# Kernel tuning notes

Measured on AMD Instinct MI355X. Metric: run time of the kernel, lower is better.

The kernel has to match this reference:

```python
import jax, jax.numpy as jnp
import numpy as np

N_NODES = 50000
N_EDGES = 800000
IN_CH = 128
CH = 128
OUT_CH = 128
N_TAPS = 3
N_LAYERS = 2


def setup_inputs() -> dict:
    key = jax.random.key(0)
    ks = jax.random.split(key, 8)
    s = 0.05
    x = jax.random.normal(ks[0], (N_NODES, IN_CH), dtype=jnp.float32)
    edge_index = jax.random.randint(ks[1], (2, N_EDGES), 0, N_NODES)
    # readin MLP: 1 layer, plain_last=False -> Linear + activation
    w_in = jax.random.normal(ks[2], (IN_CH, CH), dtype=jnp.float32) * s
    b_in = jnp.zeros((CH,), jnp.float32)
    # per-layer GraphFilter taps: (n_taps+1) Linears of [CH, CH]
    taps_w = jax.random.normal(ks[3], (N_LAYERS, N_TAPS + 1, CH, CH), dtype=jnp.float32) * s
    taps_b = jax.random.normal(ks[4], (N_LAYERS, N_TAPS + 1, CH), dtype=jnp.float32) * s
    # readout MLP: 1 layer, plain_last=True -> Linear only
    w_out = jax.random.normal(ks[5], (CH, OUT_CH), dtype=jnp.float32) * s
    b_out = jnp.zeros((OUT_CH,), jnp.float32)
    return {
        "x": x,
        "edge_index": edge_index,
        "w_in": w_in,
        "b_in": b_in,
        "taps_w": taps_w,
        "taps_b": taps_b,
        "w_out": w_out,
        "b_out": b_out,
    }


def reference(x, edge_index, w_in, b_in, taps_w, taps_b, w_out, b_out):
    act = jax.nn.leaky_relu  # torch LeakyReLU default negative_slope=0.01
    src, dst = edge_index[0], edge_index[1]
    n = x.shape[0]

    # readin: Linear + act (plain_last=False)
    h = act(x @ w_in + b_in)

    n_layers, n_taps_p1 = taps_w.shape[0], taps_w.shape[1]
    for l in range(n_layers):
        # ResidualBlock: y = act(h); y = GraphFilter(y); h = h + y
        y = act(h)
        out = y @ taps_w[l, 0] + taps_b[l, 0]
        for k in range(1, n_taps_p1):
            # SimpleConv(aggr='sum'): y_i = sum_{(s->i) in E} y_s
            y = jax.ops.segment_sum(y[src], dst, num_segments=n)
            out = out + y @ taps_w[l, k] + taps_b[l, k]
        h = h + out

    # readout: Linear only (plain_last=True)
    return h @ w_out + b_out
```

## Files before the change

### kernel.cpp

```cpp
#include <hip/hip_runtime.h>

typedef unsigned int uint;
typedef unsigned short ushort;

using bf16x8 = __attribute__((ext_vector_type(8))) short;
using f32x4  = __attribute__((ext_vector_type(4))) float;

__device__ __forceinline__ float lrelu(float v) { return v > 0.f ? v : 0.01f * v; }
__device__ __forceinline__ float b2f(ushort u) { return __uint_as_float((uint)u << 16); }
__device__ __forceinline__ ushort f2b(float f) {
  uint u = __float_as_uint(f);
  u += 0x7fffu + ((u >> 16) & 1u);
  return (ushort)(u >> 16);
}

#define CSR_B 256
#define BKT_SHIFT 10
#define MAX_NB 64

template <int MODE, int K>
__global__ __launch_bounds__(256) void gemm_mfma(
    const ushort* __restrict__ A0, const ushort* __restrict__ A1,
    const ushort* __restrict__ A2, const ushort* __restrict__ A3,
    const ushort* __restrict__ Wt, const float* __restrict__ bias,
    float* __restrict__ h, ushort* __restrict__ yout, int do_act, int N) {
  __shared__ ushort As[64][40];
  __shared__ ushort Bs[128][40];
  const int tid = threadIdx.x;
  const int lane = tid & 63;
  const int wave = tid >> 6;
  const int g = lane >> 4;
  const int mr = lane & 15;
  const int wr = wave >> 1;
  const int wc = wave & 1;
  const int row0 = blockIdx.x * 64;

  const ushort* Ap[4] = {A0, A1, A2, A3};

  f32x4 acc[2][4];
#pragma unroll
  for (int i = 0; i < 2; i++)
#pragma unroll
    for (int j = 0; j < 4; j++) acc[i][j] = (f32x4){0.f, 0.f, 0.f, 0.f};

#pragma unroll 4
  for (int kc = 0; kc < K; kc += 32) {
    {
      int m = tid >> 2, q = tid & 3;
      int r = row0 + m;
      if (r >= N) r = N - 1;
      int kg = kc + q * 8;
      const ushort* ap = Ap[kg >> 7] + (size_t)r * 128 + (kg & 127);
      *(uint4*)&As[m][q * 8] = *(const uint4*)ap;
    }
#pragma unroll
    for (int t = 0; t < 2; t++) {
      int slot = tid + t * 256;
      int n = slot >> 2, q = slot & 3;
      *(uint4*)&Bs[n][q * 8] = *(const uint4*)(Wt + (size_t)n * K + kc + q * 8);
    }
    __syncthreads();
    bf16x8 af[2], bf[4];
#pragma unroll
    for (int rt = 0; rt < 2; rt++) af[rt] = *(bf16x8*)&As[wr * 32 + rt * 16 + mr][g * 8];
#pragma unroll
    for (int ct = 0; ct < 4; ct++) bf[ct] = *(bf16x8*)&Bs[wc * 64 + ct * 16 + mr][g * 8];
#pragma unroll
    for (int rt = 0; rt < 2; rt++)
#pragma unroll
      for (int ct = 0; ct < 4; ct++)
        acc[rt][ct] = __builtin_amdgcn_mfma_f32_16x16x32_bf16(af[rt], bf[ct], acc[rt][ct], 0, 0, 0);
    __syncthreads();
  }

#pragma unroll
  for (int rt = 0; rt < 2; rt++) {
#pragma unroll
    for (int i = 0; i < 4; i++) {
      int R = row0 + wr * 32 + rt * 16 + g * 4 + i;
      if (R >= N) continue;
#pragma unroll
      for (int ct = 0; ct < 4; ct++) {
        int c = wc * 64 + ct * 16 + mr;
        float v = acc[rt][ct][i] + bias[c];
        size_t o = (size_t)R * 128 + c;
        if (MODE == 0) {
          float hv = lrelu(v);
          h[o] = hv;
          yout[o] = f2b(lrelu(hv));
        } else if (MODE == 1) {
          float hv = h[o] + v;
          h[o] = hv;
          if (yout) yout[o] = f2b(do_act ? lrelu(hv) : hv);
        } else {
          h[o] = v;
        }
      }
    }
  }
}

__global__ __launch_bounds__(256) void agg_bf16(const ushort* __restrict__ yin,
                                                ushort* __restrict__ yout,
                                                const int* __restrict__ rowp,
                                                const ushort* __restrict__ esrc, int N) {
  int t = threadIdx.x;
  int node = blockIdx.x * 16 + (t >> 4);
  if (node >= N) return;
  int lane = t & 15;
  int beg = rowp[node], end = rowp[node + 1];
  float s[8] = {0.f, 0.f, 0.f, 0.f, 0.f, 0.f, 0.f, 0.f};
  int j = beg;
  for (; j + 4 <= end; j += 4) {
    int s0 = esrc[j], s1 = esrc[j + 1], s2 = esrc[j + 2], s3 = esrc[j + 3];
    union { uint4 v; ushort u[8]; } w0, w1, w2, w3;
    w0.v = *(const uint4*)(yin + (size_t)s0 * 128 + lane * 8);
    w1.v = *(const uint4*)(yin + (size_t)s1 * 128 + lane * 8);
    w2.v = *(const uint4*)(yin + (size_t)s2 * 128 + lane * 8);
    w3.v = *(const uint4*)(yin + (size_t)s3 * 128 + lane * 8);
#pragma unroll
    for (int e = 0; e < 8; e++)
      s[e] += (b2f(w0.u[e]) + b2f(w1.u[e])) + (b2f(w2.u[e]) + b2f(w3.u[e]));
  }
  for (; j < end; j++) {
    int sn = esrc[j];
    union { uint4 v; ushort u[8]; } w;
    w.v = *(const uint4*)(yin + (size_t)sn * 128 + lane * 8);
#pragma unroll
    for (int e = 0; e < 8; e++) s[e] += b2f(w.u[e]);
  }
  union { uint4 v; ushort u[8]; } o;
#pragma unroll
  for (int e = 0; e < 8; e++) o.u[e] = f2b(s[e]);
  *(uint4*)(yout + (size_t)node * 128 + lane * 8) = o.v;
}

__global__ __launch_bounds__(256) void cast_f2b(const float* __restrict__ in,
                                                ushort* __restrict__ out, int n8) {
  int i = blockIdx.x * 256 + threadIdx.x;
  if (i >= n8) return;
  float4 a = ((const float4*)in)[i * 2];
  float4 b = ((const float4*)in)[i * 2 + 1];
  float v[8] = {a.x, a.y, a.z, a.w, b.x, b.y, b.z, b.w};
  union { uint4 q; ushort u[8]; } o;
#pragma unroll
  for (int e = 0; e < 8; e++) o.u[e] = f2b(v[e]);
  ((uint4*)out)[i] = o.q;
}

__global__ __launch_bounds__(256) void prep_k(const float* __restrict__ w_in,
                                              const float* __restrict__ w_out,
                                              const float* __restrict__ taps_w,
                                              const float* __restrict__ taps_b,
                                              ushort* __restrict__ Wt_in,
                                              ushort* __restrict__ Wt_out,
                                              ushort* __restrict__ Wt_l0,
                                              ushort* __restrict__ Wt_l1,
                                              float* __restrict__ bsum) {
  int gid = blockIdx.x * 256 + threadIdx.x;
  if (gid < 16384) {
    int n = gid >> 7, k = gid & 127;
    Wt_in[gid] = f2b(w_in[k * 128 + n]);
  } else if (gid < 32768) {
    int i = gid - 16384;
    int n = i >> 7, k = i & 127;
    Wt_out[i] = f2b(w_out[k * 128 + n]);
  } else if (gid < 98304) {
    int i = gid - 32768;
    int n = i >> 9, k = i & 511;
    Wt_l0[i] = f2b(taps_w[(size_t)k * 128 + n]);
  } else if (gid < 163840) {
    int i = gid - 98304;
    int n = i >> 9, k = i & 511;
    Wt_l1[i] = f2b(taps_w[(size_t)(512 + k) * 128 + n]);
  } else if (gid < 164096) {
    int i = gid - 163840;
    int l = i >> 7, n = i & 127;
    float s = 0.f;
    for (int k = 0; k < 4; k++) s += taps_b[l * 512 + k * 128 + n];
    bsum[i] = s;
  }
}

__global__ __launch_bounds__(256) void chist_k(const int* __restrict__ dst,
                                               int* __restrict__ H, int E, int NB) {
  __shared__ int hh[MAX_NB];
  if (threadIdx.x < NB) hh[threadIdx.x] = 0;
  __syncthreads();
  int chunk = (E + gridDim.x - 1) / gridDim.x;
  int beg = blockIdx.x * chunk, end = min(E, beg + chunk);
  for (int e = beg + threadIdx.x; e < end; e += 256)
    atomicAdd(&hh[dst[e] >> BKT_SHIFT], 1);
  __syncthreads();
  if (threadIdx.x < NB) H[threadIdx.x * gridDim.x + blockIdx.x] = hh[threadIdx.x];
}

__global__ __launch_bounds__(256) void cscan_k(int* __restrict__ H, int M) {
  __shared__ int sm[256];
  int per = (M + 255) / 256;
  int b0 = threadIdx.x * per;
  int hi = min(M, b0 + per);
  int sum = 0;
  for (int i = b0; i < hi; i++) sum += H[i];
  sm[threadIdx.x] = sum;
  __syncthreads();
  int x = sum;
  for (int off = 1; off < 256; off <<= 1) {
    int tt = (threadIdx.x >= off) ? sm[threadIdx.x - off] : 0;
    __syncthreads();
    x += tt;
    sm[threadIdx.x] = x;
    __syncthreads();
  }
  int run = x - sum;
  for (int i = b0; i < hi; i++) {
    int v = H[i];
    H[i] = run;
    run += v;
  }
}

__global__ __launch_bounds__(256) void cscatter_k(const int* __restrict__ src,
                                                  const int* __restrict__ dst,
                                                  const int* __restrict__ H,
                                                  uint* __restrict__ packed,
                                                  int E, int NB) {
  __shared__ int cur[MAX_NB];
  int chunk = (E + gridDim.x - 1) / gridDim.x;
  int beg = blockIdx.x * chunk, end = min(E, beg + chunk);
  if (threadIdx.x < NB) cur[threadIdx.x] = H[threadIdx.x * gridDim.x + blockIdx.x];
  __syncthreads();
  for (int e = beg + threadIdx.x; e < end; e += 256) {
    int d = dst[e];
    int pos = atomicAdd(&cur[d >> BKT_SHIFT], 1);
    packed[pos] = ((uint)d << 16) | (uint)src[e];
  }
}

__global__ __launch_bounds__(256) void fsort_k(const uint* __restrict__ packed,
                                               const int* __restrict__ H,
                                               ushort* __restrict__ esrc,
                                               int* __restrict__ rowp,
                                               int N, int E, int NB) {
  __shared__ int hist[1 << BKT_SHIFT];
  __shared__ int cur[1 << BKT_SHIFT];
  __shared__ int sm[256];
  const int bkt = blockIdx.x;
  const int base = bkt << BKT_SHIFT;
  const int nb_nodes = min(1 << BKT_SHIFT, N - base);
  const int start = H[bkt * CSR_B];
  const int end = (bkt == NB - 1) ? E : H[(bkt + 1) * CSR_B];

  for (int i = threadIdx.x; i < (1 << BKT_SHIFT); i += 256) hist[i] = 0;
  __syncthreads();
  for (int e = start + threadIdx.x; e < end; e += 256)
    atomicAdd(&hist[(packed[e] >> 16) - base], 1);
  __syncthreads();

  int t4 = threadIdx.x * 4;
  int l0 = hist[t4], l1 = hist[t4 + 1], l2 = hist[t4 + 2], l3 = hist[t4 + 3];
  int ssum = l0 + l1 + l2 + l3;
  sm[threadIdx.x] = ssum;
  __syncthreads();
  int x = ssum;
  for (int off = 1; off < 256; off <<= 1) {
    int tt = (threadIdx.x >= off) ? sm[threadIdx.x - off] : 0;
    __syncthreads();
    x += tt;
    sm[threadIdx.x] = x;
    __syncthreads();
  }
  int c0 = start + x - ssum;
  int c1 = c0 + l0, c2 = c1 + l1, c3 = c2 + l2;
  cur[t4] = c0; cur[t4 + 1] = c1; cur[t4 + 2] = c2; cur[t4 + 3] = c3;
  if (t4 + 0 < nb_nodes) rowp[base + t4 + 0] = c0;
  if (t4 + 1 < nb_nodes) rowp[base + t4 + 1] = c1;
  if (t4 + 2 < nb_nodes) rowp[base + t4 + 2] = c2;
  if (t4 + 3 < nb_nodes) rowp[base + t4 + 3] = c3;
  __syncthreads();

  for (int e = start + threadIdx.x; e < end; e += 256) {
    uint p = packed[e];
    int pos = atomicAdd(&cur[(p >> 16) - base], 1);
    esrc[pos] = (ushort)(p & 0xffffu);
  }
  if (bkt == 0 && threadIdx.x == 0) rowp[N] = E;
}

extern "C" void kernel_launch(void* const* d_in, const int* in_sizes, int n_in,
                              void* d_out, int out_size, void* d_ws, size_t ws_size,
                              hipStream_t stream) {
  const float* x      = (const float*)d_in[0];
  const int*   ei     = (const int*)d_in[1];
  const float* w_in   = (const float*)d_in[2];
  const float* b_in   = (const float*)d_in[3];
  const float* taps_w = (const float*)d_in[4];
  const float* taps_b = (const float*)d_in[5];
  const float* w_out  = (const float*)d_in[6];
  const float* b_out  = (const float*)d_in[7];

  const int N = in_sizes[0] / 128;
  const int E = in_sizes[1] / 2;
  const int* src = ei;
  const int* dst = ei + E;
  const int NB = (N + (1 << BKT_SHIFT) - 1) >> BKT_SHIFT;

  float* h = (float*)d_out;

  const size_t yelem = (size_t)N * 128;
  ushort* y0 = (ushort*)d_ws;
  ushort* y1 = y0 + yelem;
  ushort* y2 = y1 + yelem;
  ushort* y3 = y2 + yelem;
  ushort* Wt_in  = y3 + yelem;
  ushort* Wt_out = Wt_in + 128 * 128;
  ushort* Wt_l0  = Wt_out + 128 * 128;
  ushort* Wt_l1  = Wt_l0 + 128 * 512;
  float*  bsum   = (float*)(Wt_l1 + 128 * 512);
  int*    rowp   = (int*)(bsum + 256);
  int*    H      = rowp + (N + 1);
  uint*   packed = (uint*)(H + MAX_NB * CSR_B);
  ushort* esrc   = (ushort*)(packed + E);

  const int gemmB = (N + 63) / 64;
  const int aggB  = (N + 15) / 16;
  const int castB = (N * 16 + 255) / 256;

  chist_k<<<CSR_B, 256, 0, stream>>>(dst, H, E, NB);
  cscan_k<<<1, 256, 0, stream>>>(H, NB * CSR_B);
  cscatter_k<<<CSR_B, 256, 0, stream>>>(src, dst, H, packed, E, NB);
  fsort_k<<<NB, 256, 0, stream>>>(packed, H, esrc, rowp, N, E, NB);

  prep_k<<<641, 256, 0, stream>>>(w_in, w_out, taps_w, taps_b,
                                  Wt_in, Wt_out, Wt_l0, Wt_l1, bsum);
  cast_f2b<<<castB, 256, 0, stream>>>(x, y1, N * 16);

  gemm_mfma<0, 128><<<gemmB, 256, 0, stream>>>(y1, y1, y1, y1, Wt_in, b_in, h, y0, 0, N);

  for (int l = 0; l < 2; l++) {
    const ushort* Wt_l = (l == 0) ? Wt_l0 : Wt_l1;
    agg_bf16<<<aggB, 256, 0, stream>>>(y0, y1, rowp, esrc, N);
    agg_bf16<<<aggB, 256, 0, stream>>>(y1, y2, rowp, esrc, N);
    agg_bf16<<<aggB, 256, 0, stream>>>(y2, y3, rowp, esrc, N);
    gemm_mfma<1, 512><<<gemmB, 256, 0, stream>>>(y0, y1, y2, y3, Wt_l, bsum + l * 128,
                                                 h, y0, (l == 0) ? 1 : 0, N);
  }

  gemm_mfma<2, 128><<<gemmB, 256, 0, stream>>>(y0, y0, y0, y0, Wt_out, b_out,
                                               (float*)d_out, nullptr, 0, N);
}
```

Measured before the change: 410.0 us.

## Store bf16 node features in chunk-major 16-channel layout for cache-local gathers

Node feature buffers are reorganised from row-major [N][128] into eight chunk-major planes of [N][16], and the aggregation kernel assigns each block one channel chunk with 4 threads per node. The goal is to shrink the per-pass random-gather working set so it fits in on-chip caches. GEMM loads/stores and the input cast are adapted to the new layout. The trade-off is narrower 8-byte per-lane gathers and 32-byte row segments, which may waste cache-line bandwidth, and blocks of different chunks are interleaved rather than grouped.

```diff
diff --git a/kernel.cpp b/kernel.cpp
--- a/kernel.cpp
+++ b/kernel.cpp
@@ -17,6 +17,7 @@
 #define CSR_B 256
 #define BKT_SHIFT 10
 #define MAX_NB 64
+
 
 template <int MODE, int K>
 __global__ __launch_bounds__(256) void gemm_mfma(
@@ -50,7 +51,8 @@
       int r = row0 + m;
       if (r >= N) r = N - 1;
       int kg = kc + q * 8;
-      const ushort* ap = Ap[kg >> 7] + (size_t)r * 128 + (kg & 127);
+      const ushort* ap = Ap[kg >> 7] + ((size_t)((kg >> 4) & 7)) * N * 16 +
+                         (size_t)r * 16 + (kg & 15);
       *(uint4*)&As[m][q * 8] = *(const uint4*)ap;
     }
 #pragma unroll
@@ -84,14 +86,15 @@
         int c = wc * 64 + ct * 16 + mr;
         float v = acc[rt][ct][i] + bias[c];
         size_t o = (size_t)R * 128 + c;
+        size_t oy = (size_t)(wc * 4 + ct) * N * 16 + (size_t)R * 16 + mr;
         if (MODE == 0) {
           float hv = lrelu(v);
           h[o] = hv;
-          yout[o] = f2b(lrelu(hv));
+          yout[oy] = f2b(lrelu(hv));
         } else if (MODE == 1) {
           float hv = h[o] + v;
           h[o] = hv;
-          if (yout) yout[o] = f2b(do_act ? lrelu(hv) : hv);
+          if (yout) yout[oy] = f2b(do_act ? lrelu(hv) : hv);
         } else {
           h[o] = v;
         }
@@ -105,47 +108,51 @@
                                                 const int* __restrict__ rowp,
                                                 const ushort* __restrict__ esrc, int N) {
   int t = threadIdx.x;
-  int node = blockIdx.x * 16 + (t >> 4);
+  int chunk = blockIdx.x & 7;
+  int node = (blockIdx.x >> 3) * 64 + (t >> 2);
   if (node >= N) return;
-  int lane = t & 15;
+  int lane = t & 3;
+  const ushort* yb = yin + (size_t)chunk * N * 16 + lane * 4;
   int beg = rowp[node], end = rowp[node + 1];
-  float s[8] = {0.f, 0.f, 0.f, 0.f, 0.f, 0.f, 0.f, 0.f};
+  float s[4] = {0.f, 0.f, 0.f, 0.f};
   int j = beg;
   for (; j + 4 <= end; j += 4) {
     int s0 = esrc[j], s1 = esrc[j + 1], s2 = esrc[j + 2], s3 = esrc[j + 3];
-    union { uint4 v; ushort u[8]; } w0, w1, w2, w3;
-    w0.v = *(const uint4*)(yin + (size_t)s0 * 128 + lane * 8);
-    w1.v = *(const uint4*)(yin + (size_t)s1 * 128 + lane * 8);
-    w2.v = *(const uint4*)(yin + (size_t)s2 * 128 + lane * 8);
-    w3.v = *(const uint4*)(yin + (size_t)s3 * 128 + lane * 8);
-#pragma unroll
-    for (int e = 0; e < 8; e++)
+    union { uint2 v; ushort u[4]; } w0, w1, w2, w3;
+    w0.v = *(const uint2*)(yb + (size_t)s0 * 16);
+    w1.v = *(const uint2*)(yb + (size_t)s1 * 16);
+    w2.v = *(const uint2*)(yb + (size_t)s2 * 16);
+    w3.v = *(const uint2*)(yb + (size_t)s3 * 16);
+#pragma unroll
+    for (int e = 0; e < 4; e++)
       s[e] += (b2f(w0.u[e]) + b2f(w1.u[e])) + (b2f(w2.u[e]) + b2f(w3.u[e]));
   }
   for (; j < end; j++) {
     int sn = esrc[j];
-    union { uint4 v; ushort u[8]; } w;
-    w.v = *(const uint4*)(yin + (size_t)sn * 128 + lane * 8);
-#pragma unroll
-    for (int e = 0; e < 8; e++) s[e] += b2f(w.u[e]);
-  }
-  union { uint4 v; ushort u[8]; } o;
-#pragma unroll
-  for (int e = 0; e < 8; e++) o.u[e] = f2b(s[e]);
-  *(uint4*)(yout + (size_t)node * 128 + lane * 8) = o.v;
+    union { uint2 v; ushort u[4]; } w;
+    w.v = *(const uint2*)(yb + (size_t)sn * 16);
+#pragma unroll
+    for (int e = 0; e < 4; e++) s[e] += b2f(w.u[e]);
+  }
+  union { uint2 v; ushort u[4]; } o;
+#pragma unroll
+  for (int e = 0; e < 4; e++) o.u[e] = f2b(s[e]);
+  *(uint2*)(yout + (size_t)chunk * N * 16 + (size_t)node * 16 + lane * 4) = o.v;
 }
 
 __global__ __launch_bounds__(256) void cast_f2b(const float* __restrict__ in,
-                                                ushort* __restrict__ out, int n8) {
+                                                ushort* __restrict__ out, int N) {
   int i = blockIdx.x * 256 + threadIdx.x;
-  if (i >= n8) return;
-  float4 a = ((const float4*)in)[i * 2];
-  float4 b = ((const float4*)in)[i * 2 + 1];
+  if (i >= N * 16) return;
+  int node = i >> 4, sub = i & 15;
+  float4 a = *(const float4*)(in + (size_t)node * 128 + sub * 8);
+  float4 b = *(const float4*)(in + (size_t)node * 128 + sub * 8 + 4);
   float v[8] = {a.x, a.y, a.z, a.w, b.x, b.y, b.z, b.w};
   union { uint4 q; ushort u[8]; } o;
 #pragma unroll
   for (int e = 0; e < 8; e++) o.u[e] = f2b(v[e]);
-  ((uint4*)out)[i] = o.q;
+  int chunk = sub >> 1, off = (sub & 1) * 8;
+  *(uint4*)(out + (size_t)chunk * N * 16 + (size_t)node * 16 + off) = o.q;
 }
 
 __global__ __launch_bounds__(256) void prep_k(const float* __restrict__ w_in,
@@ -323,7 +330,7 @@
   ushort* esrc   = (ushort*)(packed + E);
 
   const int gemmB = (N + 63) / 64;
-  const int aggB  = (N + 15) / 16;
+  const int aggB  = ((N + 63) / 64) * 8;
   const int castB = (N * 16 + 255) / 256;
 
   chist_k<<<CSR_B, 256, 0, stream>>>(dst, H, E, NB);
@@ -333,7 +340,7 @@
 
   prep_k<<<641, 256, 0, stream>>>(w_in, w_out, taps_w, taps_b,
                                   Wt_in, Wt_out, Wt_l0, Wt_l1, bsum);
-  cast_f2b<<<castB, 256, 0, stream>>>(x, y1, N * 16);
+  cast_f2b<<<castB, 256, 0, stream>>>(x, y1, N);
 
   gemm_mfma<0, 128><<<gemmB, 256, 0, stream>>>(y1, y1, y1, y1, Wt_in, b_in, h, y0, 0, N);
 
```

Measured after the change: 450.1 us. 1.1x slower.

## Store bf16 activations in 32-column chunked layout for cache-friendly gathers

Applied to the files above, without the earlier changes.

Activation buffers switch from row-major [N][128] to four column chunks of [N][32], and GEMM loads/stores, the cast kernel and the aggregation kernel are updated to match. Each aggregation block now handles one 64-byte chunk for 64 nodes, so concurrently running blocks gather from a 3.2 MB working set that fits in L2, instead of the full 12.8 MB feature matrix. In exchange, each gather is only 64 bytes per edge, edge indices are re-read once per chunk, and GEMM A-loads and epilogue stores become more strided.

```diff
diff --git a/kernel.cpp b/kernel.cpp
--- a/kernel.cpp
+++ b/kernel.cpp
@@ -17,6 +17,7 @@
 #define CSR_B 256
 #define BKT_SHIFT 10
 #define MAX_NB 64
+
 
 template <int MODE, int K>
 __global__ __launch_bounds__(256) void gemm_mfma(
@@ -50,7 +51,8 @@
       int r = row0 + m;
       if (r >= N) r = N - 1;
       int kg = kc + q * 8;
-      const ushort* ap = Ap[kg >> 7] + (size_t)r * 128 + (kg & 127);
+      const ushort* ap = Ap[kg >> 7] + ((size_t)((kg >> 5) & 3)) * N * 32 +
+                         (size_t)r * 32 + (kg & 31);
       *(uint4*)&As[m][q * 8] = *(const uint4*)ap;
     }
 #pragma unroll
@@ -84,14 +86,15 @@
         int c = wc * 64 + ct * 16 + mr;
         float v = acc[rt][ct][i] + bias[c];
         size_t o = (size_t)R * 128 + c;
+        size_t oy = (size_t)(c >> 5) * N * 32 + (size_t)R * 32 + (c & 31);
         if (MODE == 0) {
           float hv = lrelu(v);
           h[o] = hv;
-          yout[o] = f2b(lrelu(hv));
+          yout[oy] = f2b(lrelu(hv));
         } else if (MODE == 1) {
           float hv = h[o] + v;
           h[o] = hv;
-          if (yout) yout[o] = f2b(do_act ? lrelu(hv) : hv);
+          if (yout) yout[oy] = f2b(do_act ? lrelu(hv) : hv);
         } else {
           h[o] = v;
         }
@@ -105,19 +108,21 @@
                                                 const int* __restrict__ rowp,
                                                 const ushort* __restrict__ esrc, int N) {
   int t = threadIdx.x;
-  int node = blockIdx.x * 16 + (t >> 4);
+  int chunk = blockIdx.x & 3;
+  int node = (blockIdx.x >> 2) * 64 + (t >> 2);
   if (node >= N) return;
-  int lane = t & 15;
+  int lane = t & 3;
+  const ushort* yb = yin + (size_t)chunk * N * 32 + lane * 8;
   int beg = rowp[node], end = rowp[node + 1];
   float s[8] = {0.f, 0.f, 0.f, 0.f, 0.f, 0.f, 0.f, 0.f};
   int j = beg;
   for (; j + 4 <= end; j += 4) {
     int s0 = esrc[j], s1 = esrc[j + 1], s2 = esrc[j + 2], s3 = esrc[j + 3];
     union { uint4 v; ushort u[8]; } w0, w1, w2, w3;
-    w0.v = *(const uint4*)(yin + (size_t)s0 * 128 + lane * 8);
-    w1.v = *(const uint4*)(yin + (size_t)s1 * 128 + lane * 8);
-    w2.v = *(const uint4*)(yin + (size_t)s2 * 128 + lane * 8);
-    w3.v = *(const uint4*)(yin + (size_t)s3 * 128 + lane * 8);
+    w0.v = *(const uint4*)(yb + (size_t)s0 * 32);
+    w1.v = *(const uint4*)(yb + (size_t)s1 * 32);
+    w2.v = *(const uint4*)(yb + (size_t)s2 * 32);
+    w3.v = *(const uint4*)(yb + (size_t)s3 * 32);
 #pragma unroll
     for (int e = 0; e < 8; e++)
       s[e] += (b2f(w0.u[e]) + b2f(w1.u[e])) + (b2f(w2.u[e]) + b2f(w3.u[e]));
@@ -125,27 +130,29 @@
   for (; j < end; j++) {
     int sn = esrc[j];
     union { uint4 v; ushort u[8]; } w;
-    w.v = *(const uint4*)(yin + (size_t)sn * 128 + lane * 8);
+    w.v = *(const uint4*)(yb + (size_t)sn * 32);
 #pragma unroll
     for (int e = 0; e < 8; e++) s[e] += b2f(w.u[e]);
   }
   union { uint4 v; ushort u[8]; } o;
 #pragma unroll
   for (int e = 0; e < 8; e++) o.u[e] = f2b(s[e]);
-  *(uint4*)(yout + (size_t)node * 128 + lane * 8) = o.v;
+  *(uint4*)(yout + (size_t)chunk * N * 32 + (size_t)node * 32 + lane * 8) = o.v;
 }
 
 __global__ __launch_bounds__(256) void cast_f2b(const float* __restrict__ in,
-                                                ushort* __restrict__ out, int n8) {
+                                                ushort* __restrict__ out, int N) {
   int i = blockIdx.x * 256 + threadIdx.x;
-  if (i >= n8) return;
-  float4 a = ((const float4*)in)[i * 2];
-  float4 b = ((const float4*)in)[i * 2 + 1];
+  if (i >= N * 16) return;
+  int node = i >> 4, sub = i & 15;
+  float4 a = *(const float4*)(in + (size_t)node * 128 + sub * 8);
+  float4 b = *(const float4*)(in + (size_t)node * 128 + sub * 8 + 4);
   float v[8] = {a.x, a.y, a.z, a.w, b.x, b.y, b.z, b.w};
   union { uint4 q; ushort u[8]; } o;
 #pragma unroll
   for (int e = 0; e < 8; e++) o.u[e] = f2b(v[e]);
-  ((uint4*)out)[i] = o.q;
+  int chunk = sub >> 2, off = (sub & 3) * 8;
+  *(uint4*)(out + (size_t)chunk * N * 32 + (size_t)node * 32 + off) = o.q;
 }
 
 __global__ __launch_bounds__(256) void prep_k(const float* __restrict__ w_in,
@@ -323,7 +330,7 @@
   ushort* esrc   = (ushort*)(packed + E);
 
   const int gemmB = (N + 63) / 64;
-  const int aggB  = (N + 15) / 16;
+  const int aggB  = ((N + 63) / 64) * 4;
   const int castB = (N * 16 + 255) / 256;
 
   chist_k<<<CSR_B, 256, 0, stream>>>(dst, H, E, NB);
@@ -333,7 +340,7 @@
 
   prep_k<<<641, 256, 0, stream>>>(w_in, w_out, taps_w, taps_b,
                                   Wt_in, Wt_out, Wt_l0, Wt_l1, bsum);
-  cast_f2b<<<castB, 256, 0, stream>>>(x, y1, N * 16);
+  cast_f2b<<<castB, 256, 0, stream>>>(x, y1, N);
 
   gemm_mfma<0, 128><<<gemmB, 256, 0, stream>>>(y1, y1, y1, y1, Wt_in, b_in, h, y0, 0, N);
 
```

After: 391.8 us. 1.05x faster.
